# Kernel optimization log

Measured on AMD Instinct MI355X. Metric: run time of the kernel, lower is better.

The kernel has to match this reference:

```python
import jax, jax.numpy as jnp
import numpy as np
from jax import lax

B, C, L, K = 8, 256, 4096, 65
PAD = K // 2  # torch: int(kernel.shape[-1] / 2) = 32 -> same-length output for odd K


def depthwise_corr(x, k):
    """Depthwise cross-correlation (torch conv1d semantics, no kernel flip).
    x: [B, C, L] float32, k: [K] float32 (same kernel shared by all channels,
    matching kernel.repeat(seq_len, 1)). Returns [B, C, L]."""
    w = jnp.broadcast_to(k.reshape(1, 1, K), (C, 1, K))  # [C, 1, K]
    return lax.conv_general_dilated(
        x, w, window_strides=(1,), padding=[(PAD, PAD)],
        dimension_numbers=("NCH", "OIH", "NCH"), feature_group_count=C)


def setup_inputs() -> dict:
    key = jax.random.key(0)
    k1, k2, k3 = jax.random.split(key, 3)
    return {
        "x": jax.random.normal(k1, (B, C, L), dtype=jnp.float32),
        "kernel_real": jax.random.normal(k2, (K,), dtype=jnp.float32),
        "kernel_imag": jax.random.normal(k3, (K,), dtype=jnp.float32),
        "weights_mag": jnp.ones((1, C, 1), dtype=jnp.float32),
        "weights_angle": jnp.ones((1, C, 1), dtype=jnp.float32),
    }


def reference(x, kernel_real, kernel_imag, weights_mag, weights_angle):
    # mf_coeffs = conj(kernel) -> weight = kernel_real - 1j*kernel_imag.
    # Input x is real (imag=0 after .to(complex64)), so complex conv splits
    # into two real depthwise correlations.
    yr = depthwise_corr(x, kernel_real)            # [B, C, L]
    yi = -depthwise_corr(x, kernel_imag)           # [B, C, L]
    y = lax.complex(yr, yi)                        # complex64 [B, C, L]

    # torch.std over dims (1,2), unbiased (correction=1), complex -> real std
    mean = jnp.mean(y, axis=(1, 2), keepdims=True)
    n = C * L
    var = jnp.sum(jnp.abs(y - mean) ** 2, axis=(1, 2), keepdims=True) / (n - 1)
    y = y / jnp.sqrt(var)                          # real std broadcasts over complex

    # weights_mag * y * exp(-1j * weights_angle)
    phase = lax.complex(jnp.cos(weights_angle), -jnp.sin(weights_angle))  # [1, C, 1]
    y = weights_mag * y * phase

    # FFT over the channel dim (dim=-2), then fftshift on that dim
    return jnp.fft.fftshift(jnp.fft.fft(y, axis=-2), axes=-2)
```

## Files before the change

### kernel.cpp

```cpp
#include <hip/hip_runtime.h>
#include <math.h>

#define NB 8
#define NC 256
#define NL 4096
#define NK 65
#define NSL (NL / 16)

typedef float vf4 __attribute__((ext_vector_type(4)));
typedef float vf2 __attribute__((ext_vector_type(2)));

__device__ float4 g_part[NB * NSL];

__device__ __forceinline__ int lidx(int row, int q) {
    return (row << 3) + (q ^ (row & 7));
}

#define PKFMA_EVEN(ACC, WP, K2)                                             \
    asm("v_pk_fma_f32 %0, %1, %2, %0 op_sel:[0,0,0] op_sel_hi:[0,1,1]"      \
        : "+v"(ACC) : "v"(WP), "v"(K2))
#define PKFMA_ODD(ACC, WP, K2)                                              \
    asm("v_pk_fma_f32 %0, %1, %2, %0 op_sel:[1,0,0] op_sel_hi:[1,1,1]"      \
        : "+v"(ACC) : "v"(WP), "v"(K2))

#define LOAD16P(W2, off)                                                    \
    {                                                                       \
        const int g0_ = l0 + (off);                                         \
        if (g0_ >= 0 && g0_ + 16 <= NL) {         \
            _Pragma("unroll")                                               \
            for (int q = 0; q < 4; ++q) {                                   \
                const float4 v_ = *(const float4*)(xr + g0_ + 4 * q);       \
                vf2 a_; a_.x = v_.x; a_.y = v_.y; W2[2*q]   = a_;           \
                vf2 b_; b_.x = v_.z; b_.y = v_.w; W2[2*q+1] = b_;           \
            }                                                               \
        } else {                                                            \
            _Pragma("unroll")                                               \
            for (int q = 0; q < 8; ++q) {                                   \
                const int g_ = g0_ + 2 * q;                                 \
                vf2 a_;                                                     \
                a_.x = (g_     >= 0 && g_     < NL) ? xr[g_]     : 0.0f;    \
                a_.y = (g_ + 1 >= 0 && g_ + 1 < NL) ? xr[g_ + 1] : 0.0f;    \
                W2[q] = a_;                                                 \
            }                                                               \
        }                                                                   \
    }

#define CHUNK16PK(LoP, HiP, tb)                                             \
    {                                                                       \
        _Pragma("unroll")                                                   \
        for (int j2 = 0; j2 < 16; ++j2) {                                   \
            vf2 k2_; k2_.x = kre[(tb) + j2]; k2_.y = kim[(tb) + j2];        \
            _Pragma("unroll")                                               \
            for (int i = 0; i < 16; ++i) {                                  \
                const int w_ = i + j2;                                      \
                const int p_ = w_ >> 1;                                     \
                vf2 wp_ = (p_ < 8) ? LoP[p_] : HiP[p_ - 8];                 \
                if ((w_ & 1) == 0) { PKFMA_EVEN(s2[i], wp_, k2_); }         \
                else               { PKFMA_ODD (s2[i], wp_, k2_); }         \
            }                                                               \
        }                                                                   \
    }

__device__ __forceinline__ int digitrev_shift(int pp) {
    int k = ((pp & 3) << 6) | (((pp >> 2) & 3) << 4)
          | (((pp >> 4) & 3) << 2) | ((pp >> 6) & 3);
    return k ^ 128;
}

__global__ __launch_bounds__(256, 4) void fused_conv_fft_kernel(
    const float* __restrict__ x,
    const float* __restrict__ kre,
    const float* __restrict__ kim,
    const float* __restrict__ wmag,
    const float* __restrict__ wang,
    float* __restrict__ out,
    int out_size)
{
    __shared__ __align__(16) float4 lbuf4[NC * 9];

    const int t = threadIdx.x;
    const int b = blockIdx.x & 7;
    const int st = blockIdx.x >> 3;
    const int l0 = st << 4;
    const int lane = t & 63, wv = t >> 6;

    const float* xr = x + (size_t)b * NC * NL + (size_t)t * NL;
    const bool interleaved = (out_size >= 2 * NB * NC * NL);

    vf2 s2[16];
    #pragma unroll
    for (int i = 0; i < 16; ++i) { s2[i].x = 0.0f; s2[i].y = 0.0f; }

    vf2 W0[8], W1[8], W2[8], W3[8];
    LOAD16P(W0, -32);
    LOAD16P(W1, -16);
    LOAD16P(W2, 0);
    LOAD16P(W3, 16);
    CHUNK16PK(W0, W1, 0);
    LOAD16P(W0, 32);
    CHUNK16PK(W1, W2, 16);
    CHUNK16PK(W2, W3, 32);
    CHUNK16PK(W3, W0, 48);
    {
        vf2 k2_; k2_.x = kre[64]; k2_.y = kim[64];
        #pragma unroll
        for (int i = 0; i < 16; ++i) {
            vf2 wp_ = W0[i >> 1];
            if ((i & 1) == 0) { PKFMA_EVEN(s2[i], wp_, k2_); }
            else              { PKFMA_ODD (s2[i], wp_, k2_); }
        }
    }

    vf2 tsum; tsum.x = 0.0f; tsum.y = 0.0f;
    vf2 tsq2; tsq2.x = 0.0f; tsq2.y = 0.0f;
    #pragma unroll
    for (int i = 0; i < 16; ++i) {
        tsum = tsum + s2[i];
        tsq2 = __builtin_elementwise_fma(s2[i], s2[i], tsq2);
    }
    float tsr = tsum.x, tsi = -tsum.y, tsq = tsq2.x + tsq2.y;

    float sw, cw;
    sincosf(wang[t], &sw, &cw);
    const float wm = wmag[t];
    const float wgr =  wm * cw;
    const float wgi = -wm * sw;
    float tw64r, tw64i;
    {
        float ang = (float)lane * 0.024543692606170260f;
        float s, c;
        sincosf(ang, &s, &c);
        tw64r = c; tw64i = -s;
    }

    #pragma unroll
    for (int k = 0; k < 8; ++k) {
        float srA = s2[2*k].x,   siA = s2[2*k].y;
        float srB = s2[2*k+1].x, siB = s2[2*k+1].y;
        float4 o;
        o.x = srA * wgr + siA * wgi;
        o.y = srA * wgi - siA * wgr;
        o.z = srB * wgr + siB * wgi;
        o.w = srB * wgi - siB * wgr;
        lbuf4[lidx(t, k)] = o;
    }
    __syncthreads();

    #pragma unroll
    for (int s = 0; s < 3; ++s) {
        const int shift = 2 * s;
        const int q = 64 >> shift;
        #pragma unroll
        for (int it = 0; it < 2; ++it) {
            int task = it * 256 + t;
            int lpp = task & 7;
            int m = task >> 3;
            int j = m & (q - 1);
            int blk = m >> (6 - shift);
            int base2 = blk << (8 - shift);

            int ca = base2 + j;
            float4 a0 = lbuf4[lidx(ca, lpp)];
            float4 a1 = lbuf4[lidx(ca + q, lpp)];
            float4 a2 = lbuf4[lidx(ca + 2*q, lpp)];
            float4 a3 = lbuf4[lidx(ca + 3*q, lpp)];

            int e = j << shift;
            float w1r = __shfl(tw64r, e);
            float w1i = __shfl(tw64i, e);
            float w2r = fmaf(w1r, w1r, -(w1i * w1i));
            float w2i = 2.0f * w1r * w1i;
            float w3r = w2r * w1r - w2i * w1i;
            float w3i = w2r * w1i + w2i * w1r;

            float4 b0, b1, b2, b3;
            {
                float t0r = a0.x + a2.x, t0i = a0.y + a2.y;
                float t1r = a0.x - a2.x, t1i = a0.y - a2.y;
                float t2r = a1.x + a3.x, t2i = a1.y + a3.y;
                float t3r = a1.x - a3.x, t3i = a1.y - a3.y;
                b0.x = t0r + t2r;       b0.y = t0i + t2i;
                float b2r = t0r - t2r,  b2i = t0i - t2i;
                float b1r = t1r + t3i,  b1i = t1i - t3r;
                float b3r = t1r - t3i,  b3i = t1i + t3r;
                b1.x = b1r*w1r - b1i*w1i;  b1.y = b1r*w1i + b1i*w1r;
                b2.x = b2r*w2r - b2i*w2i;  b2.y = b2r*w2i + b2i*w2r;
                b3.x = b3r*w3r - b3i*w3i;  b3.y = b3r*w3i + b3i*w3r;
            }
            {
                float t0r = a0.z + a2.z, t0i = a0.w + a2.w;
                float t1r = a0.z - a2.z, t1i = a0.w - a2.w;
                float t2r = a1.z + a3.z, t2i = a1.w + a3.w;
                float t3r = a1.z - a3.z, t3i = a1.w - a3.w;
                b0.z = t0r + t2r;       b0.w = t0i + t2i;
                float b2r = t0r - t2r,  b2i = t0i - t2i;
                float b1r = t1r + t3i,  b1i = t1i - t3r;
                float b3r = t1r - t3i,  b3i = t1i + t3r;
                b1.z = b1r*w1r - b1i*w1i;  b1.w = b1r*w1i + b1i*w1r;
                b2.z = b2r*w2r - b2i*w2i;  b2.w = b2r*w2i + b2i*w2r;
                b3.z = b3r*w3r - b3i*w3i;  b3.w = b3r*w3i + b3i*w3r;
            }
            lbuf4[lidx(ca, lpp)]         = b0;
            lbuf4[lidx(ca + q, lpp)]     = b1;
            lbuf4[lidx(ca + 2*q, lpp)]   = b2;
            lbuf4[lidx(ca + 3*q, lpp)]   = b3;
        }
        __syncthreads();
    }

    #pragma unroll
    for (int it = 0; it < 2; ++it) {
        int task = it * 256 + t;
        int lpp = task & 7;
        int m = task >> 3;
        int ca = m << 2;
        float4 a0 = lbuf4[lidx(ca + 0, lpp)];
        float4 a1 = lbuf4[lidx(ca + 1, lpp)];
        float4 a2 = lbuf4[lidx(ca + 2, lpp)];
        float4 a3 = lbuf4[lidx(ca + 3, lpp)];

        float4 b0, b1, b2, b3;
        {
            float t0r = a0.x + a2.x, t0i = a0.y + a2.y;
            float t1r = a0.x - a2.x, t1i = a0.y - a2.y;
            float t2r = a1.x + a3.x, t2i = a1.y + a3.y;
            float t3r = a1.x - a3.x, t3i = a1.y - a3.y;
            b0.x = t0r + t2r;  b0.y = t0i + t2i;
            b2.x = t0r - t2r;  b2.y = t0i - t2i;
            b1.x = t1r + t3i;  b1.y = t1i - t3r;
            b3.x = t1r - t3i;  b3.y = t1i + t3r;
        }
        {
            float t0r = a0.z + a2.z, t0i = a0.w + a2.w;
            float t1r = a0.z - a2.z, t1i = a0.w - a2.w;
            float t2r = a1.z + a3.z, t2i = a1.w + a3.w;
            float t3r = a1.z - a3.z, t3i = a1.w - a3.w;
            b0.z = t0r + t2r;  b0.w = t0i + t2i;
            b2.z = t0r - t2r;  b2.w = t0i - t2i;
            b1.z = t1r + t3i;  b1.w = t1i - t3r;
            b3.z = t1r - t3i;  b3.w = t1i + t3r;
        }

        float4 bb[4] = { b0, b1, b2, b3 };
        #pragma unroll
        for (int mm = 0; mm < 4; ++mm) {
            int cout = digitrev_shift(ca + mm);
            float4 v = bb[mm];
            if (interleaved) {
                size_t fi = 2 * ((size_t)(b * NC + cout) * NL + l0) + 4 * lpp;
                if (fi + 4 <= (size_t)out_size) {
                    *(float4*)(out + fi) = v;
                }
            } else {
                size_t fi = (size_t)(b * NC + cout) * NL + l0 + 2 * lpp;
                if (fi + 2 <= (size_t)out_size) {
                    float2 o2; o2.x = v.x; o2.y = v.z;
                    *(float2*)(out + fi) = o2;
                }
            }
        }
    }

    #pragma unroll
    for (int off = 32; off > 0; off >>= 1) {
        tsr += __shfl_down(tsr, off);
        tsi += __shfl_down(tsi, off);
        tsq += __shfl_down(tsq, off);
    }
    __syncthreads();
    float* redf = (float*)lbuf4;
    if (lane == 0) { redf[wv*3+0] = tsr; redf[wv*3+1] = tsi; redf[wv*3+2] = tsq; }
    __syncthreads();
    if (t == 0) {
        float a0 = 0.0f, a1 = 0.0f, a2 = 0.0f;
        #pragma unroll
        for (int i = 0; i < 4; ++i) { a0 += redf[i*3]; a1 += redf[i*3+1]; a2 += redf[i*3+2]; }
        g_part[b * NSL + st] = make_float4(a0, a1, a2, 0.0f);
    }
}

__global__ __launch_bounds__(256) void scale_out_kernel(
    float* __restrict__ out, int out_size)
{
    __shared__ float sred[13];
    const int t = threadIdx.x;
    const int j = blockIdx.x;
    const int b = j & 7;
    const int seg = j >> 3;
    const int lane = t & 63, wv = t >> 6;

    float4 p = g_part[b * NSL + t];
    float psr = p.x, psi = p.y, psq = p.z;
    #pragma unroll
    for (int off = 32; off > 0; off >>= 1) {
        psr += __shfl_down(psr, off);
        psi += __shfl_down(psi, off);
        psq += __shfl_down(psq, off);
    }
    if (lane == 0) { sred[wv*3+0] = psr; sred[wv*3+1] = psi; sred[wv*3+2] = psq; }
    __syncthreads();
    if (t == 0) {
        float a0 = 0.0f, a1 = 0.0f, a2 = 0.0f;
        #pragma unroll
        for (int i = 0; i < 4; ++i) { a0 += sred[i*3]; a1 += sred[i*3+1]; a2 += sred[i*3+2]; }
        const float n = (float)(NC * NL);
        float var = (a2 - (a0*a0 + a1*a1)/n) / (n - 1.0f);
        sred[12] = rsqrtf(var);
    }
    __syncthreads();
    const float inv = sred[12];

    const int fpbatch = out_size >> 3;
    const int fpseg = fpbatch >> 8;
    const int base = b * fpbatch + seg * fpseg;
    if ((fpseg & 3) == 0 && ((size_t)(out + base) & 15) == 0) {
        float4* o4 = (float4*)(out + base);
        const int n4 = fpseg >> 2;
        for (int i = t; i < n4; i += 256) {
            float4 v = o4[i];
            v.x *= inv; v.y *= inv; v.z *= inv; v.w *= inv;
            o4[i] = v;
        }
    } else {
        for (int i = t; i < fpseg; i += 256) out[base + i] *= inv;
    }
    if (j == 2047) {
        for (int i = ((out_size >> 11) << 11) + t; i < out_size; i += 256)
            out[i] *= inv;
    }
}

extern "C" void kernel_launch(void* const* d_in, const int* in_sizes, int n_in,
                              void* d_out, int out_size, void* d_ws, size_t ws_size,
                              hipStream_t stream)
{
    const float* x   = (const float*)d_in[0];
    const float* kre = (const float*)d_in[1];
    const float* kim = (const float*)d_in[2];
    const float* wm  = (const float*)d_in[3];
    const float* wa  = (const float*)d_in[4];
    float* out = (float*)d_out;
    (void)d_ws; (void)ws_size;

    fused_conv_fft_kernel<<<NB * NSL, 256, 0, stream>>>(x, kre, kim, wm, wa,
                                                        out, out_size);
    scale_out_kernel<<<2048, 256, 0, stream>>>(out, out_size);
}
```

Measured before the change: 134.3 us.

## Fuse conv-FFT and normalization into one cooperative kernel with grid sync

Replaces the two-kernel sequence (conv+FFT, then a global scale pass) with one cooperative kernel of 1024 blocks, each handling two 16-column tiles. Blocks write per-batch partial statistics, meet at a grid-wide sync, reduce the variance locally, then rescale the output they just wrote, which is likely still in cache. This removes a second launch and a separate full read/write pass over the output, at the cost of a grid barrier and fewer, longer-running blocks. If cooperative launch fails, the old two-kernel path is used.

```diff
diff --git a/kernel.cpp b/kernel.cpp
--- a/kernel.cpp
+++ b/kernel.cpp
@@ -1,11 +1,15 @@
 #include <hip/hip_runtime.h>
+#include <hip/hip_cooperative_groups.h>
 #include <math.h>
+
+namespace cg = cooperative_groups;
 
 #define NB 8
 #define NC 256
 #define NL 4096
 #define NK 65
 #define NSL (NL / 16)
+#define NSP 128
 
 typedef float vf4 __attribute__((ext_vector_type(4)));
 typedef float vf2 __attribute__((ext_vector_type(2)));
@@ -67,26 +71,14 @@
     return k ^ 128;
 }
 
-__global__ __launch_bounds__(256, 4) void fused_conv_fft_kernel(
-    const float* __restrict__ x,
+__device__ __forceinline__ void do_tile(
+    const float* __restrict__ xr,
     const float* __restrict__ kre,
     const float* __restrict__ kim,
-    const float* __restrict__ wmag,
-    const float* __restrict__ wang,
-    float* __restrict__ out,
-    int out_size)
+    float wgr, float wgi, float tw64r, float tw64i,
+    int l0, int b, float* __restrict__ out, int out_size, bool interleaved,
+    float4* lbuf4, int t, float& tsr, float& tsi, float& tsq)
 {
-    __shared__ __align__(16) float4 lbuf4[NC * 9];
-
-    const int t = threadIdx.x;
-    const int b = blockIdx.x & 7;
-    const int st = blockIdx.x >> 3;
-    const int l0 = st << 4;
-    const int lane = t & 63, wv = t >> 6;
-
-    const float* xr = x + (size_t)b * NC * NL + (size_t)t * NL;
-    const bool interleaved = (out_size >= 2 * NB * NC * NL);
-
     vf2 s2[16];
     #pragma unroll
     for (int i = 0; i < 16; ++i) { s2[i].x = 0.0f; s2[i].y = 0.0f; }
@@ -118,20 +110,9 @@
         tsum = tsum + s2[i];
         tsq2 = __builtin_elementwise_fma(s2[i], s2[i], tsq2);
     }
-    float tsr = tsum.x, tsi = -tsum.y, tsq = tsq2.x + tsq2.y;
-
-    float sw, cw;
-    sincosf(wang[t], &sw, &cw);
-    const float wm = wmag[t];
-    const float wgr =  wm * cw;
-    const float wgi = -wm * sw;
-    float tw64r, tw64i;
-    {
-        float ang = (float)lane * 0.024543692606170260f;
-        float s, c;
-        sincosf(ang, &s, &c);
-        tw64r = c; tw64i = -s;
-    }
+    tsr += tsum.x; tsi -= tsum.y; tsq += tsq2.x + tsq2.y;
+
+    __syncthreads();
 
     #pragma unroll
     for (int k = 0; k < 8; ++k) {
@@ -260,6 +241,153 @@
             }
         }
     }
+}
+
+__global__ __launch_bounds__(256, 4) void fused_all_kernel(
+    const float* __restrict__ x,
+    const float* __restrict__ kre,
+    const float* __restrict__ kim,
+    const float* __restrict__ wmag,
+    const float* __restrict__ wang,
+    float* __restrict__ out,
+    int out_size)
+{
+    __shared__ __align__(16) float4 lbuf4[NC * 9];
+
+    const int t = threadIdx.x;
+    const int b = blockIdx.x & 7;
+    const int sp = blockIdx.x >> 3;
+    const int l0A = sp << 5;
+    const int l0B = l0A + 16;
+    const int lane = t & 63, wv = t >> 6;
+
+    const float* xr = x + (size_t)b * NC * NL + (size_t)t * NL;
+    const bool interleaved = (out_size >= 2 * NB * NC * NL);
+
+    float sw, cw;
+    sincosf(wang[t], &sw, &cw);
+    const float wm = wmag[t];
+    const float wgr =  wm * cw;
+    const float wgi = -wm * sw;
+    float tw64r, tw64i;
+    {
+        float ang = (float)lane * 0.024543692606170260f;
+        float s, c;
+        sincosf(ang, &s, &c);
+        tw64r = c; tw64i = -s;
+    }
+
+    float tsr = 0.0f, tsi = 0.0f, tsq = 0.0f;
+    do_tile(xr, kre, kim, wgr, wgi, tw64r, tw64i, l0A, b, out, out_size,
+            interleaved, lbuf4, t, tsr, tsi, tsq);
+    do_tile(xr, kre, kim, wgr, wgi, tw64r, tw64i, l0B, b, out, out_size,
+            interleaved, lbuf4, t, tsr, tsi, tsq);
+
+    #pragma unroll
+    for (int off = 32; off > 0; off >>= 1) {
+        tsr += __shfl_down(tsr, off);
+        tsi += __shfl_down(tsi, off);
+        tsq += __shfl_down(tsq, off);
+    }
+    __syncthreads();
+    float* redf = (float*)lbuf4;
+    if (lane == 0) { redf[wv*3+0] = tsr; redf[wv*3+1] = tsi; redf[wv*3+2] = tsq; }
+    __syncthreads();
+    if (t == 0) {
+        float a0 = 0.0f, a1 = 0.0f, a2 = 0.0f;
+        #pragma unroll
+        for (int i = 0; i < 4; ++i) { a0 += redf[i*3]; a1 += redf[i*3+1]; a2 += redf[i*3+2]; }
+        g_part[b * NSP + sp] = make_float4(a0, a1, a2, 0.0f);
+        __threadfence();
+    }
+
+    cg::this_grid().sync();
+
+    float psr = 0.0f, psi = 0.0f, psq = 0.0f;
+    if (t < NSP) {
+        float4 p = g_part[b * NSP + t];
+        psr = p.x; psi = p.y; psq = p.z;
+    }
+    #pragma unroll
+    for (int off = 32; off > 0; off >>= 1) {
+        psr += __shfl_down(psr, off);
+        psi += __shfl_down(psi, off);
+        psq += __shfl_down(psq, off);
+    }
+    if (wv < 2 && lane == 0) { redf[wv*3+0] = psr; redf[wv*3+1] = psi; redf[wv*3+2] = psq; }
+    __syncthreads();
+    if (t == 0) {
+        float a0 = redf[0] + redf[3], a1 = redf[1] + redf[4], a2 = redf[2] + redf[5];
+        const float n = (float)(NC * NL);
+        float var = (a2 - (a0*a0 + a1*a1)/n) / (n - 1.0f);
+        redf[0] = rsqrtf(var);
+    }
+    __syncthreads();
+    const float inv = redf[0];
+
+    if (interleaved) {
+        #pragma unroll
+        for (int it = 0; it < 16; ++it) {
+            int task = it * 256 + t;
+            int row = task >> 4, q = task & 15;
+            size_t fi = 2 * ((size_t)(b * NC + row) * NL + l0A) + 4 * q;
+            if (fi + 4 <= (size_t)out_size) {
+                float4 v = *(float4*)(out + fi);
+                v.x *= inv; v.y *= inv; v.z *= inv; v.w *= inv;
+                *(float4*)(out + fi) = v;
+            }
+        }
+    } else {
+        #pragma unroll
+        for (int it = 0; it < 8; ++it) {
+            int task = it * 256 + t;
+            int row = task >> 3, q = task & 7;
+            size_t fi = (size_t)(b * NC + row) * NL + l0A + 4 * q;
+            if (fi + 4 <= (size_t)out_size) {
+                float4 v = *(float4*)(out + fi);
+                v.x *= inv; v.y *= inv; v.z *= inv; v.w *= inv;
+                *(float4*)(out + fi) = v;
+            }
+        }
+    }
+}
+
+__global__ __launch_bounds__(256, 4) void fused_conv_fft_kernel(
+    const float* __restrict__ x,
+    const float* __restrict__ kre,
+    const float* __restrict__ kim,
+    const float* __restrict__ wmag,
+    const float* __restrict__ wang,
+    float* __restrict__ out,
+    int out_size)
+{
+    __shared__ __align__(16) float4 lbuf4[NC * 9];
+
+    const int t = threadIdx.x;
+    const int b = blockIdx.x & 7;
+    const int st = blockIdx.x >> 3;
+    const int l0 = st << 4;
+    const int lane = t & 63, wv = t >> 6;
+
+    const float* xr = x + (size_t)b * NC * NL + (size_t)t * NL;
+    const bool interleaved = (out_size >= 2 * NB * NC * NL);
+
+    float sw, cw;
+    sincosf(wang[t], &sw, &cw);
+    const float wm = wmag[t];
+    const float wgr =  wm * cw;
+    const float wgi = -wm * sw;
+    float tw64r, tw64i;
+    {
+        float ang = (float)lane * 0.024543692606170260f;
+        float s, c;
+        sincosf(ang, &s, &c);
+        tw64r = c; tw64i = -s;
+    }
+
+    float tsr = 0.0f, tsi = 0.0f, tsq = 0.0f;
+    do_tile(xr, kre, kim, wgr, wgi, tw64r, tw64i, l0, b, out, out_size,
+            interleaved, lbuf4, t, tsr, tsi, tsq);
 
     #pragma unroll
     for (int off = 32; off > 0; off >>= 1) {
@@ -342,7 +470,16 @@
     float* out = (float*)d_out;
     (void)d_ws; (void)ws_size;
 
-    fused_conv_fft_kernel<<<NB * NSL, 256, 0, stream>>>(x, kre, kim, wm, wa,
-                                                        out, out_size);
-    scale_out_kernel<<<2048, 256, 0, stream>>>(out, out_size);
-}
+    void* args[7] = { (void*)&x, (void*)&kre, (void*)&kim, (void*)&wm,
+                      (void*)&wa, (void*)&out, (void*)&out_size };
+    hipError_t e = hipLaunchCooperativeKernel(
+        (const void*)fused_all_kernel, dim3(NB * NSP), dim3(256),
+        args, 0, stream);
+
+    if (e != hipSuccess) {
+        (void)hipGetLastError();
+        fused_conv_fft_kernel<<<NB * NSL, 256, 0, stream>>>(
+            x, kre, kim, wm, wa, out, out_size);
+        scale_out_kernel<<<2048, 256, 0, stream>>>(out, out_size);
+    }
+}
```

Measured after the change: 357.2 us. +165.9%, slower.
